# Optimization experiments

Measured on AMD Instinct MI355X. Metric: run time of the kernel, lower is better.

The kernel has to match this reference:

```python
import jax, jax.numpy as jnp
import numpy as np

EPS = 1e-6  # torch F.pairwise_distance default eps added to the difference


def setup_inputs() -> dict:
    key = jax.random.key(0)
    k1, k2 = jax.random.split(key)
    x = jax.random.normal(k1, (8, 4096, 512), dtype=jnp.float32)
    centroids = jax.random.normal(k2, (2048, 512), dtype=jnp.float32)
    return {"x": x, "centroids": centroids}


def reference(x, centroids):
    # Faithful to KMeans.forward with normalize=None, p_norm=2, return_centroids=True.
    # torch pairwise_distance computes ||x - c + eps||_2; expand algebraically with
    # xe = x + eps to avoid materializing the (b, k, d) broadcast:
    #   ||xe - c||^2 = ||xe||^2 - 2 xe.c + ||c||^2
    batch_shape = x.shape[:-1]
    d = x.shape[-1]
    xf = x.reshape(-1, d)                    # (b, d)
    xe = xf + EPS
    x_sq = jnp.sum(xe * xe, axis=-1, keepdims=True)          # (b, 1)
    c_sq = jnp.sum(centroids * centroids, axis=-1)[None, :]  # (1, k)
    sq = x_sq + c_sq - 2.0 * (xe @ centroids.T)              # (b, k)
    dist = jnp.sqrt(jnp.maximum(sq, 0.0))
    labels = jnp.argmin(dist, axis=-1)                        # (b,)
    assigned = centroids[labels]                              # (b, d)
    labels = labels.reshape(batch_shape)
    assigned = assigned.reshape(*batch_shape, d)
    return labels, assigned
```

## Files before the change

kernel.cpp:

```cpp
#include <hip/hip_runtime.h>
#include <hip/hip_bf16.h>


#define EPS 1e-6f
#define TAU 0.3f

constexpr int BROWS = 32768;
constexpr int DD    = 512;
constexpr int KC    = 2048;
constexpr int FCAP  = 4096;

typedef _Float16 half8  __attribute__((ext_vector_type(8)));
typedef _Float16 half4v __attribute__((ext_vector_type(4)));
typedef float    f32x4  __attribute__((ext_vector_type(4)));

__global__ __launch_bounds__(256) void prep_x(const float* __restrict__ x,
                                              _Float16* __restrict__ xh) {
    size_t i = ((size_t)blockIdx.x * 256 + threadIdx.x) * 4;
    float4 v = *(const float4*)(x + i);
    half4v h;
    h[0] = (_Float16)(v.x + EPS); h[1] = (_Float16)(v.y + EPS);
    h[2] = (_Float16)(v.z + EPS); h[3] = (_Float16)(v.w + EPS);
    *(half4v*)(xh + i) = h;
}

__global__ __launch_bounds__(256) void prep_c(const float* __restrict__ cen,
                                              _Float16* __restrict__ ch,
                                              float* __restrict__ csq) {
    int w = threadIdx.x >> 6, lane = threadIdx.x & 63;
    int c = blockIdx.x * 4 + w;
    const float* row = cen + (size_t)c * DD;
    float4 v0 = *(const float4*)(row + lane * 8);
    float4 v1 = *(const float4*)(row + lane * 8 + 4);
    half8 h;
    h[0] = (_Float16)v0.x; h[1] = (_Float16)v0.y; h[2] = (_Float16)v0.z; h[3] = (_Float16)v0.w;
    h[4] = (_Float16)v1.x; h[5] = (_Float16)v1.y; h[6] = (_Float16)v1.z; h[7] = (_Float16)v1.w;
    *(half8*)(ch + (size_t)c * DD + lane * 8) = h;
    float s = v0.x*v0.x + v0.y*v0.y + v0.z*v0.z + v0.w*v0.w
            + v1.x*v1.x + v1.y*v1.y + v1.z*v1.z + v1.w*v1.w;
    #pragma unroll
    for (int off = 32; off > 0; off >>= 1) s += __shfl_down(s, off, 64);
    if (lane == 0) csq[c] = s;
}

__global__ __launch_bounds__(256, 4) void dist_f16(const _Float16* __restrict__ xh,
                                                   const _Float16* __restrict__ ch,
                                                   const float* __restrict__ csq,
                                                   float* __restrict__ pbest,
                                                   float* __restrict__ psec,
                                                   int*   __restrict__ pidx) {
    __shared__ __align__(16) _Float16 ash[2][128 * 32];
    __shared__ __align__(16) _Float16 bsh[2][128 * 32];

    const int tid = threadIdx.x;
    const int w = tid >> 6, lane = tid & 63;
    const int wr = w >> 1, wc = w & 1;
    const int quad = lane >> 4, u = lane & 15;
    const int rowBase = blockIdx.x * 128;
    const int colBase = blockIdx.y * 128;

    const int g0 = 128 * w + lane;
    const int g1 = g0 + 64;
    const int r0 = g0 >> 2, h0 = g0 & 3;
    const int r1 = g1 >> 2, h1 = g1 & 3;
    const _Float16* pa0 = xh + (size_t)(rowBase + r0) * DD + h0 * 8;
    const _Float16* pa1 = xh + (size_t)(rowBase + r1) * DD + h1 * 8;
    const _Float16* pb0 = ch + (size_t)(colBase + r0) * DD + h0 * 8;
    const _Float16* pb1 = ch + (size_t)(colBase + r1) * DD + h1 * 8;

    auto stage = [&](int buf, int kt) {
        const int off = kt * 32;
        __builtin_amdgcn_global_load_lds(
            (const __attribute__((address_space(1))) void*)(pa0 + off),
            (__attribute__((address_space(3))) void*)(&ash[buf][g0 * 8]), 16, 0, 0);
        __builtin_amdgcn_global_load_lds(
            (const __attribute__((address_space(1))) void*)(pb0 + off),
            (__attribute__((address_space(3))) void*)(&bsh[buf][g0 * 8]), 16, 0, 0);
        __builtin_amdgcn_global_load_lds(
            (const __attribute__((address_space(1))) void*)(pa1 + off),
            (__attribute__((address_space(3))) void*)(&ash[buf][g1 * 8]), 16, 0, 0);
        __builtin_amdgcn_global_load_lds(
            (const __attribute__((address_space(1))) void*)(pb1 + off),
            (__attribute__((address_space(3))) void*)(&bsh[buf][g1 * 8]), 16, 0, 0);
    };

    f32x4 acc[4][4] = {};

    stage(0, 0);
    __syncthreads();

    for (int kc = 0; kc < DD / 32; kc++) {
        const int cur = kc & 1;
        if (kc + 1 < DD / 32) stage(cur ^ 1, kc + 1);

        half8 af[4], bf[4];
        #pragma unroll
        for (int f = 0; f < 4; f++) {
            af[f] = *(const half8*)(&ash[cur][(wr * 64 + f * 16 + u) * 32 + quad * 8]);
            bf[f] = *(const half8*)(&bsh[cur][(wc * 64 + f * 16 + u) * 32 + quad * 8]);
        }
        #pragma unroll
        for (int fr = 0; fr < 4; fr++)
            #pragma unroll
            for (int fc = 0; fc < 4; fc++)
                acc[fr][fc] = __builtin_amdgcn_mfma_f32_16x16x32_f16(af[fr], bf[fc], acc[fr][fc], 0, 0, 0);

        __syncthreads();
    }

    float cq[4];
    #pragma unroll
    for (int fc = 0; fc < 4; fc++) cq[fc] = csq[colBase + wc * 64 + fc * 16 + u];
    const int cbi = blockIdx.y * 2 + wc;
    const int colQuadBase = colBase + wc * 64;

    #pragma unroll
    for (int fr = 0; fr < 4; fr++) {
        #pragma unroll
        for (int reg = 0; reg < 4; reg++) {
            float vv[4];
            #pragma unroll
            for (int fc = 0; fc < 4; fc++) vv[fc] = cq[fc] - 2.0f * acc[fr][fc][reg];
            float mn01 = fminf(vv[0], vv[1]), mx01 = fmaxf(vv[0], vv[1]);
            float mn23 = fminf(vv[2], vv[3]), mx23 = fmaxf(vv[2], vv[3]);
            float b = fminf(mn01, mn23);
            float s = fminf(fmaxf(mn01, mn23), fminf(mx01, mx23));
            #pragma unroll
            for (int m = 1; m < 16; m <<= 1) {
                float ob = __shfl_xor(b, m, 64);
                float os = __shfl_xor(s, m, 64);
                s = fminf(fminf(s, os), fmaxf(b, ob));
                b = fminf(b, ob);
            }
            int bi = 0x7fffffff;
            #pragma unroll
            for (int fc = 0; fc < 4; fc++) {
                unsigned long long mm = __ballot(vv[fc] == b);
                unsigned q16 = (unsigned)((mm >> (quad * 16)) & 0xFFFFu);
                if (bi == 0x7fffffff && q16)
                    bi = colQuadBase + fc * 16 + (__ffs(q16) - 1);
            }
            if (u == 0) {
                int grow = rowBase + wr * 64 + fr * 16 + quad * 4 + reg;
                pbest[cbi * BROWS + grow] = b;
                psec [cbi * BROWS + grow] = s;
                pidx [cbi * BROWS + grow] = bi;
            }
        }
    }
}

__global__ __launch_bounds__(256) void reduce_rows(const float* __restrict__ pbest,
                                                   const float* __restrict__ psec,
                                                   const int* __restrict__ pidx,
                                                   float* __restrict__ out,
                                                   int* __restrict__ labels,
                                                   int* __restrict__ rlist,
                                                   int* __restrict__ ctr) {
    int row = blockIdx.x * 256 + threadIdx.x;
    float b = 3.4e38f, s = 3.4e38f; int bi = 0x7fffffff;
    for (int p = 0; p < 32; p++) {
        float v  = pbest[p * BROWS + row];
        float sv = psec [p * BROWS + row];
        int   vi = pidx [p * BROWS + row];
        if (v < b) { s = fminf(b, fminf(s, sv)); b = v; bi = vi; }
        else       { s = fminf(s, fminf(v, sv)); }
    }
    out[row] = (float)bi;
    labels[row] = bi;
    if (s - b < TAU) {
        int slot = atomicAdd(ctr, 1);
        if (slot < FCAP) rlist[slot] = row;
    }
}

__global__ __launch_bounds__(256, 2) void fixup_dist(const float* __restrict__ x,
                                                     const float* __restrict__ cen,
                                                     const float* __restrict__ csq,
                                                     const int* __restrict__ rlist,
                                                     const int* __restrict__ ctr,
                                                     float* __restrict__ fbest,
                                                     int*   __restrict__ fidx) {
    int n = min(*ctr, FCAP);
    int tilebase = blockIdx.y * 128;
    if (tilebase >= n) return;

    __shared__ float xs[16][132];
    __shared__ float cs[16][132];
    __shared__ float redv[128][17];
    __shared__ int   redi[128][17];
    __shared__ int   rows[128];

    const int tid = threadIdx.x;
    if (tid < 128) rows[tid] = rlist[tilebase + tid];
    __syncthreads();

    const int ty = tid >> 4, tx = tid & 15;
    const int colBase = blockIdx.x * 128;

    float acc[8][8] = {};
    for (int dk = 0; dk < DD; dk += 16) {
        #pragma unroll
        for (int sI = 0; sI < 2; sI++) {
            int id = tid + sI * 256;
            int r  = id >> 2;
            int dc = (id & 3) * 4;
            float4 xv = *(const float4*)(x + (size_t)rows[r] * DD + dk + dc);
            xs[dc + 0][r] = xv.x + EPS; xs[dc + 1][r] = xv.y + EPS;
            xs[dc + 2][r] = xv.z + EPS; xs[dc + 3][r] = xv.w + EPS;
            float4 cv = *(const float4*)(cen + (size_t)(colBase + r) * DD + dk + dc);
            cs[dc + 0][r] = cv.x; cs[dc + 1][r] = cv.y;
            cs[dc + 2][r] = cv.z; cs[dc + 3][r] = cv.w;
        }
        __syncthreads();
        #pragma unroll
        for (int k = 0; k < 16; k++) {
            float4 a0 = *(const float4*)&xs[k][ty * 4];
            float4 a1 = *(const float4*)&xs[k][64 + ty * 4];
            float4 b0 = *(const float4*)&cs[k][tx * 4];
            float4 b1 = *(const float4*)&cs[k][64 + tx * 4];
            float a[8] = {a0.x, a0.y, a0.z, a0.w, a1.x, a1.y, a1.z, a1.w};
            float b[8] = {b0.x, b0.y, b0.z, b0.w, b1.x, b1.y, b1.z, b1.w};
            #pragma unroll
            for (int i = 0; i < 8; i++)
                #pragma unroll
                for (int j = 0; j < 8; j++)
                    acc[i][j] += a[i] * b[j];
        }
        __syncthreads();
    }

    float bv[8]; int bix[8];
    #pragma unroll
    for (int i = 0; i < 8; i++) { bv[i] = 3.4e38f; bix[i] = 0x7fffffff; }
    #pragma unroll
    for (int j = 0; j < 8; j++) {
        int col = colBase + ((j < 4) ? (tx * 4 + j) : (64 + tx * 4 + (j - 4)));
        float cq = csq[col];
        #pragma unroll
        for (int i = 0; i < 8; i++) {
            float v = cq - 2.0f * acc[i][j];
            if (v < bv[i] || (v == bv[i] && col < bix[i])) { bv[i] = v; bix[i] = col; }
        }
    }
    #pragma unroll
    for (int i = 0; i < 8; i++) {
        int r = (i < 4) ? (ty * 4 + i) : (64 + ty * 4 + (i - 4));
        redv[r][tx] = bv[i]; redi[r][tx] = bix[i];
    }
    __syncthreads();
    if (tid < 128) {
        float b = 3.4e38f; int bi = 0x7fffffff;
        #pragma unroll
        for (int t = 0; t < 16; t++) {
            float v = redv[tid][t]; int ix = redi[tid][t];
            if (v < b || (v == b && ix < bi)) { b = v; bi = ix; }
        }
        fbest[blockIdx.x * FCAP + tilebase + tid] = b;
        fidx [blockIdx.x * FCAP + tilebase + tid] = bi;
    }
}

__global__ __launch_bounds__(256) void fixup_reduce(const float* __restrict__ fbest,
                                                    const int* __restrict__ fidx,
                                                    const int* __restrict__ rlist,
                                                    const int* __restrict__ ctr,
                                                    float* __restrict__ out,
                                                    int* __restrict__ labels) {
    int s = blockIdx.x * 256 + threadIdx.x;
    int n = min(*ctr, FCAP);
    if (s >= n) return;
    float b = 3.4e38f; int bi = 0x7fffffff;
    for (int c = 0; c < 16; c++) {
        float v = fbest[c * FCAP + s]; int ix = fidx[c * FCAP + s];
        if (v < b || (v == b && ix < bi)) { b = v; bi = ix; }
    }
    int row = rlist[s];
    out[row] = (float)bi;
    labels[row] = bi;
}

__global__ __launch_bounds__(256) void gather(const float* __restrict__ cen,
                                              const int* __restrict__ labels,
                                              float* __restrict__ out) {
    __shared__ int lab[8];
    const int tid = threadIdx.x;
    const int rowBase = blockIdx.x * 8;
    if (tid < 8) lab[tid] = labels[rowBase + tid];
    __syncthreads();
    float* assigned = out + BROWS;
    #pragma unroll 4
    for (int s = tid; s < 8 * 128; s += 256) {
        int r = s >> 7;
        int f = (s & 127) * 4;
        float4 v = *(const float4*)(cen + (size_t)lab[r] * DD + f);
        *(float4*)(assigned + (size_t)(rowBase + r) * DD + f) = v;
    }
}

extern "C" void kernel_launch(void* const* d_in, const int* in_sizes, int n_in,
                              void* d_out, int out_size, void* d_ws, size_t ws_size,
                              hipStream_t stream) {
    const float* x   = (const float*)d_in[0];
    const float* cen = (const float*)d_in[1];

    char* base = (char*)d_ws;
    _Float16* xh   = (_Float16*)(base);
    _Float16* ch   = (_Float16*)(base + 33554432);
    float* csq     = (float*)(base + 35651584);
    float* pbest   = (float*)(base + 35659776);
    float* psec    = (float*)(base + 39854080);
    int*   pidx    = (int*)  (base + 44048384);
    int*   labels  = (int*)  (base + 48242688);
    int*   rlist   = (int*)  (base + 48373760);
    float* fbest   = (float*)(base + 48390144);
    int*   fidx    = (int*)  (base + 48652288);
    int*   ctr     = (int*)  (base + 48914432);

    hipMemsetAsync(ctr, 0, 4, stream);
    hipMemsetAsync(rlist, 0, FCAP * 4, stream);

    prep_x<<<BROWS * DD / 4 / 256, 256, 0, stream>>>(x, xh);
    prep_c<<<KC / 4, 256, 0, stream>>>(cen, ch, csq);
    dist_f16<<<dim3(BROWS / 128, KC / 128), 256, 0, stream>>>(xh, ch, csq, pbest, psec, pidx);
    reduce_rows<<<BROWS / 256, 256, 0, stream>>>(pbest, psec, pidx, (float*)d_out, labels, rlist, ctr);
    fixup_dist<<<dim3(KC / 128, FCAP / 128), 256, 0, stream>>>(x, cen, csq, rlist, ctr, fbest, fidx);
    fixup_reduce<<<FCAP / 256, 256, 0, stream>>>(fbest, fidx, rlist, ctr, (float*)d_out, labels);
    gather<<<BROWS / 8, 256, 0, stream>>>(cen, labels, (float*)d_out);
}
```

Baseline: 336.0 us.

## Enlarge distance GEMM tile to 256 rows and stage partial argmin via LDS

```diff
diff --git a/kernel.cpp b/kernel.cpp
--- a/kernel.cpp
+++ b/kernel.cpp
@@ -43,48 +43,58 @@
     if (lane == 0) csq[c] = s;
 }
 
-__global__ __launch_bounds__(256, 4) void dist_f16(const _Float16* __restrict__ xh,
+__global__ __launch_bounds__(256, 2) void dist_f16(const _Float16* __restrict__ xh,
                                                    const _Float16* __restrict__ ch,
                                                    const float* __restrict__ csq,
                                                    float* __restrict__ pbest,
                                                    float* __restrict__ psec,
                                                    int*   __restrict__ pidx) {
-    __shared__ __align__(16) _Float16 ash[2][128 * 32];
+    __shared__ __align__(16) _Float16 ash[2][256 * 32];
     __shared__ __align__(16) _Float16 bsh[2][128 * 32];
+    __shared__ float eb[4][128];
+    __shared__ float es[4][128];
+    __shared__ int   ei[4][128];
 
     const int tid = threadIdx.x;
     const int w = tid >> 6, lane = tid & 63;
     const int wr = w >> 1, wc = w & 1;
     const int quad = lane >> 4, u = lane & 15;
-    const int rowBase = blockIdx.x * 128;
+    const int rowBase = blockIdx.x * 256;
     const int colBase = blockIdx.y * 128;
 
-    const int g0 = 128 * w + lane;
-    const int g1 = g0 + 64;
-    const int r0 = g0 >> 2, h0 = g0 & 3;
-    const int r1 = g1 >> 2, h1 = g1 & 3;
-    const _Float16* pa0 = xh + (size_t)(rowBase + r0) * DD + h0 * 8;
-    const _Float16* pa1 = xh + (size_t)(rowBase + r1) * DD + h1 * 8;
-    const _Float16* pb0 = ch + (size_t)(colBase + r0) * DD + h0 * 8;
-    const _Float16* pb1 = ch + (size_t)(colBase + r1) * DD + h1 * 8;
+    const _Float16* gA[4];
+    const _Float16* gB[2];
+    int ldsA[4], ldsB[2];
+    #pragma unroll
+    for (int j = 0; j < 4; j++) {
+        int g = w * 256 + j * 64 + lane;
+        int r = g >> 2, h = g & 3;
+        gA[j] = xh + (size_t)(rowBase + r) * DD + h * 8;
+        ldsA[j] = g * 8;
+    }
+    #pragma unroll
+    for (int j = 0; j < 2; j++) {
+        int g = w * 128 + j * 64 + lane;
+        int r = g >> 2, h = g & 3;
+        gB[j] = ch + (size_t)(colBase + r) * DD + h * 8;
+        ldsB[j] = g * 8;
+    }
 
     auto stage = [&](int buf, int kt) {
         const int off = kt * 32;
-        __builtin_amdgcn_global_load_lds(
-            (const __attribute__((address_space(1))) void*)(pa0 + off),
-            (__attribute__((address_space(3))) void*)(&ash[buf][g0 * 8]), 16, 0, 0);
-        __builtin_amdgcn_global_load_lds(
-            (const __attribute__((address_space(1))) void*)(pb0 + off),
-            (__attribute__((address_space(3))) void*)(&bsh[buf][g0 * 8]), 16, 0, 0);
-        __builtin_amdgcn_global_load_lds(
-            (const __attribute__((address_space(1))) void*)(pa1 + off),
-            (__attribute__((address_space(3))) void*)(&ash[buf][g1 * 8]), 16, 0, 0);
-        __builtin_amdgcn_global_load_lds(
-            (const __attribute__((address_space(1))) void*)(pb1 + off),
-            (__attribute__((address_space(3))) void*)(&bsh[buf][g1 * 8]), 16, 0, 0);
+        #pragma unroll
+        for (int j = 0; j < 4; j++)
+            __builtin_amdgcn_global_load_lds(
+                (const __attribute__((address_space(1))) void*)(gA[j] + off),
+                (__attribute__((address_space(3))) void*)(&ash[buf][ldsA[j]]), 16, 0, 0);
+        #pragma unroll
+        for (int j = 0; j < 2; j++)
+            __builtin_amdgcn_global_load_lds(
+                (const __attribute__((address_space(1))) void*)(gB[j] + off),
+                (__attribute__((address_space(3))) void*)(&bsh[buf][ldsB[j]]), 16, 0, 0);
     };
 
-    f32x4 acc[4][4] = {};
+    f32x4 acc[8][4] = {};
 
     stage(0, 0);
     __syncthreads();
@@ -93,14 +103,16 @@
         const int cur = kc & 1;
         if (kc + 1 < DD / 32) stage(cur ^ 1, kc + 1);
 
-        half8 af[4], bf[4];
-        #pragma unroll
-        for (int f = 0; f < 4; f++) {
-            af[f] = *(const half8*)(&ash[cur][(wr * 64 + f * 16 + u) * 32 + quad * 8]);
+        half8 af[8], bf[4];
+        #pragma unroll
+        for (int f = 0; f < 8; f++)
+            af[f] = *(const half8*)(&ash[cur][(wr * 128 + f * 16 + u) * 32 + quad * 8]);
+        #pragma unroll
+        for (int f = 0; f < 4; f++)
             bf[f] = *(const half8*)(&bsh[cur][(wc * 64 + f * 16 + u) * 32 + quad * 8]);
-        }
-        #pragma unroll
-        for (int fr = 0; fr < 4; fr++)
+
+        #pragma unroll
+        for (int fr = 0; fr < 8; fr++)
             #pragma unroll
             for (int fc = 0; fc < 4; fc++)
                 acc[fr][fc] = __builtin_amdgcn_mfma_f32_16x16x32_f16(af[fr], bf[fc], acc[fr][fc], 0, 0, 0);
@@ -115,7 +127,7 @@
     const int colQuadBase = colBase + wc * 64;
 
     #pragma unroll
-    for (int fr = 0; fr < 4; fr++) {
+    for (int fr = 0; fr < 8; fr++) {
         #pragma unroll
         for (int reg = 0; reg < 4; reg++) {
             float vv[4];
@@ -141,12 +153,20 @@
                     bi = colQuadBase + fc * 16 + (__ffs(q16) - 1);
             }
             if (u == 0) {
-                int grow = rowBase + wr * 64 + fr * 16 + quad * 4 + reg;
-                pbest[cbi * BROWS + grow] = b;
-                psec [cbi * BROWS + grow] = s;
-                pidx [cbi * BROWS + grow] = bi;
+                int rl = fr * 16 + quad * 4 + reg;
+                eb[w][rl] = b; es[w][rl] = s; ei[w][rl] = bi;
             }
         }
+    }
+    __syncthreads();
+    {
+        const int base = cbi * BROWS + rowBase + wr * 128;
+        pbest[base + lane]      = eb[w][lane];
+        pbest[base + 64 + lane] = eb[w][64 + lane];
+        psec [base + lane]      = es[w][lane];
+        psec [base + 64 + lane] = es[w][64 + lane];
+        pidx [base + lane]      = ei[w][lane];
+        pidx [base + 64 + lane] = ei[w][64 + lane];
     }
 }
 
@@ -322,7 +342,7 @@
 
     prep_x<<<BROWS * DD / 4 / 256, 256, 0, stream>>>(x, xh);
     prep_c<<<KC / 4, 256, 0, stream>>>(cen, ch, csq);
-    dist_f16<<<dim3(BROWS / 128, KC / 128), 256, 0, stream>>>(xh, ch, csq, pbest, psec, pidx);
+    dist_f16<<<dim3(BROWS / 256, KC / 128), 256, 0, stream>>>(xh, ch, csq, pbest, psec, pidx);
     reduce_rows<<<BROWS / 256, 256, 0, stream>>>(pbest, psec, pidx, (float*)d_out, labels, rlist, ctr);
     fixup_dist<<<dim3(KC / 128, FCAP / 128), 256, 0, stream>>>(x, cen, csq, rlist, ctr, fbest, fidx);
     fixup_reduce<<<FCAP / 256, 256, 0, stream>>>(fbest, fidx, rlist, ctr, (float*)d_out, labels);
```

Measured after the change: 333.9 us. No clear change (-0.6%).

## Triple-buffer A tiles with vmcnt waits and coalesce partial-result stores via LDS

Applied to the files above, without the earlier changes.

```diff
diff --git a/kernel.cpp b/kernel.cpp
--- a/kernel.cpp
+++ b/kernel.cpp
@@ -9,6 +9,7 @@
 constexpr int DD    = 512;
 constexpr int KC    = 2048;
 constexpr int FCAP  = 4096;
+constexpr int NK    = DD / 32;
 
 typedef _Float16 half8  __attribute__((ext_vector_type(8)));
 typedef _Float16 half4v __attribute__((ext_vector_type(4)));
@@ -49,8 +50,7 @@
                                                    float* __restrict__ pbest,
                                                    float* __restrict__ psec,
                                                    int*   __restrict__ pidx) {
-    __shared__ __align__(16) _Float16 ash[2][128 * 32];
-    __shared__ __align__(16) _Float16 bsh[2][128 * 32];
+    __shared__ __align__(16) _Float16 smem[5 * 4096];
 
     const int tid = threadIdx.x;
     const int w = tid >> 6, lane = tid & 63;
@@ -58,6 +58,10 @@
     const int quad = lane >> 4, u = lane & 15;
     const int rowBase = blockIdx.x * 128;
     const int colBase = blockIdx.y * 128;
+
+    float cq[4];
+    #pragma unroll
+    for (int fc = 0; fc < 4; fc++) cq[fc] = csq[colBase + wc * 64 + fc * 16 + u];
 
     const int g0 = 128 * w + lane;
     const int g1 = g0 + 64;
@@ -68,49 +72,63 @@
     const _Float16* pb0 = ch + (size_t)(colBase + r0) * DD + h0 * 8;
     const _Float16* pb1 = ch + (size_t)(colBase + r1) * DD + h1 * 8;
 
-    auto stage = [&](int buf, int kt) {
+    auto stageA = [&](int kt) {
+        _Float16* dst = smem + (kt % 3) * 4096;
         const int off = kt * 32;
         __builtin_amdgcn_global_load_lds(
             (const __attribute__((address_space(1))) void*)(pa0 + off),
-            (__attribute__((address_space(3))) void*)(&ash[buf][g0 * 8]), 16, 0, 0);
+            (__attribute__((address_space(3))) void*)(dst + g0 * 8), 16, 0, 0);
+        __builtin_amdgcn_global_load_lds(
+            (const __attribute__((address_space(1))) void*)(pa1 + off),
+            (__attribute__((address_space(3))) void*)(dst + g1 * 8), 16, 0, 0);
+    };
+    auto stageB = [&](int kt) {
+        _Float16* dst = smem + 12288 + (kt % 2) * 4096;
+        const int off = kt * 32;
         __builtin_amdgcn_global_load_lds(
             (const __attribute__((address_space(1))) void*)(pb0 + off),
-            (__attribute__((address_space(3))) void*)(&bsh[buf][g0 * 8]), 16, 0, 0);
-        __builtin_amdgcn_global_load_lds(
-            (const __attribute__((address_space(1))) void*)(pa1 + off),
-            (__attribute__((address_space(3))) void*)(&ash[buf][g1 * 8]), 16, 0, 0);
+            (__attribute__((address_space(3))) void*)(dst + g0 * 8), 16, 0, 0);
         __builtin_amdgcn_global_load_lds(
             (const __attribute__((address_space(1))) void*)(pb1 + off),
-            (__attribute__((address_space(3))) void*)(&bsh[buf][g1 * 8]), 16, 0, 0);
+            (__attribute__((address_space(3))) void*)(dst + g1 * 8), 16, 0, 0);
     };
 
     f32x4 acc[4][4] = {};
 
-    stage(0, 0);
-    __syncthreads();
-
-    for (int kc = 0; kc < DD / 32; kc++) {
-        const int cur = kc & 1;
-        if (kc + 1 < DD / 32) stage(cur ^ 1, kc + 1);
-
+    stageA(0); stageB(0); stageA(1);
+
+    #pragma unroll
+    for (int kc = 0; kc < NK; kc++) {
+        if (kc + 1 < NK) asm volatile("s_waitcnt vmcnt(2)" ::: "memory");
+        else             asm volatile("s_waitcnt vmcnt(0)" ::: "memory");
+        __builtin_amdgcn_s_barrier();
+        asm volatile("" ::: "memory");
+        __builtin_amdgcn_sched_barrier(0);
+
+        if (kc + 1 < NK) stageB(kc + 1);
+        if (kc + 2 < NK) stageA(kc + 2);
+
+        const _Float16* abuf = smem + (kc % 3) * 4096;
+        const _Float16* bbuf = smem + 12288 + (kc % 2) * 4096;
         half8 af[4], bf[4];
         #pragma unroll
         for (int f = 0; f < 4; f++) {
-            af[f] = *(const half8*)(&ash[cur][(wr * 64 + f * 16 + u) * 32 + quad * 8]);
-            bf[f] = *(const half8*)(&bsh[cur][(wc * 64 + f * 16 + u) * 32 + quad * 8]);
+            af[f] = *(const half8*)(abuf + (wr * 64 + f * 16 + u) * 32 + quad * 8);
+            bf[f] = *(const half8*)(bbuf + (wc * 64 + f * 16 + u) * 32 + quad * 8);
         }
         #pragma unroll
         for (int fr = 0; fr < 4; fr++)
             #pragma unroll
             for (int fc = 0; fc < 4; fc++)
                 acc[fr][fc] = __builtin_amdgcn_mfma_f32_16x16x32_f16(af[fr], bf[fc], acc[fr][fc], 0, 0, 0);
-
-        __syncthreads();
-    }
-
-    float cq[4];
-    #pragma unroll
-    for (int fc = 0; fc < 4; fc++) cq[fc] = csq[colBase + wc * 64 + fc * 16 + u];
+    }
+
+    __syncthreads();
+
+    float* ebf = (float*)smem;
+    float* esf = ebf + 256;
+    int*   eif = (int*)(esf + 256);
+
     const int cbi = blockIdx.y * 2 + wc;
     const int colQuadBase = colBase + wc * 64;
 
@@ -141,12 +159,17 @@
                     bi = colQuadBase + fc * 16 + (__ffs(q16) - 1);
             }
             if (u == 0) {
-                int grow = rowBase + wr * 64 + fr * 16 + quad * 4 + reg;
-                pbest[cbi * BROWS + grow] = b;
-                psec [cbi * BROWS + grow] = s;
-                pidx [cbi * BROWS + grow] = bi;
+                int rl = fr * 16 + quad * 4 + reg;
+                ebf[w * 64 + rl] = b; esf[w * 64 + rl] = s; eif[w * 64 + rl] = bi;
             }
         }
+    }
+    __syncthreads();
+    {
+        const int base = cbi * BROWS + rowBase + wr * 64;
+        pbest[base + lane] = ebf[w * 64 + lane];
+        psec [base + lane] = esf[w * 64 + lane];
+        pidx [base + lane] = eif[w * 64 + lane];
     }
 }
 
```

New measurement: 311.7 us. 1.08x faster.
